# Kernel optimization log

Hardware: AMD Instinct MI355X
Metric: run time of the kernel (lower is better)

The kernel has to match this reference:

```python
import jax, jax.numpy as jnp
import numpy as np

B, P, ENC = 64, 196, 2048
A = H = E = 512
V = 30000
L = 30  # max caption length; T = L-1 decode steps


def setup_inputs() -> dict:
    key = jax.random.key(0)
    ks = jax.random.split(key, 24)
    s = 0.02
    lengths = jax.random.randint(ks[1], (B, 1), 2, L + 1)
    lengths = lengths.at[0, 0].set(L)  # ensure max length present
    return {
        "encoder_out": jax.random.normal(ks[0], (B, P, ENC), dtype=jnp.float32),
        "enc_att_w": jax.random.normal(ks[2], (A, ENC), jnp.float32) * s,
        "enc_att_b": jnp.zeros((A,), jnp.float32),
        "dec_att_w": jax.random.normal(ks[3], (A, H), jnp.float32) * s,
        "dec_att_b": jnp.zeros((A,), jnp.float32),
        "full_att_w": jax.random.normal(ks[4], (1, A), jnp.float32) * s,
        "full_att_b": jnp.zeros((1,), jnp.float32),
        "embed": jax.random.uniform(ks[5], (V, E), jnp.float32, -0.1, 0.1),
        "W_ih": jax.random.normal(ks[6], (4 * H, E + ENC), jnp.float32) * s,
        "W_hh": jax.random.normal(ks[7], (4 * H, H), jnp.float32) * s,
        "b_ih": jnp.zeros((4 * H,), jnp.float32),
        "b_hh": jnp.zeros((4 * H,), jnp.float32),
        "init_h_w": jax.random.normal(ks[8], (H, ENC), jnp.float32) * s,
        "init_h_b": jnp.zeros((H,), jnp.float32),
        "init_c_w": jax.random.normal(ks[9], (H, ENC), jnp.float32) * s,
        "init_c_b": jnp.zeros((H,), jnp.float32),
        "f_beta_w": jax.random.normal(ks[10], (ENC, H), jnp.float32) * s,
        "f_beta_b": jnp.zeros((ENC,), jnp.float32),
        "fc_w": jax.random.uniform(ks[11], (V, H), jnp.float32, -0.1, 0.1),
        "fc_b": jnp.zeros((V,), jnp.float32),
        "encoded_captions": jax.random.randint(ks[12], (B, L), 0, V),
        "caption_lengths": lengths,
    }


def reference(encoder_out, enc_att_w, enc_att_b, dec_att_w, dec_att_b, full_att_w,
              full_att_b, embed, W_ih, W_hh, b_ih, b_hh, init_h_w, init_h_b,
              init_c_w, init_c_b, f_beta_w, f_beta_b, fc_w, fc_b,
              encoded_captions, caption_lengths):
    # sort by caption length descending (as in the torch module)
    lengths = caption_lengths[:, 0]
    sort_ind = jnp.argsort(-lengths)
    lengths = lengths[sort_ind]
    enc = encoder_out[sort_ind]               # [B,P,ENC]
    caps = encoded_captions[sort_ind]         # [B,L]
    embeds = embed[caps]                      # [B,L,E]

    mean_enc = enc.mean(axis=1)
    h0 = mean_enc @ init_h_w.T + init_h_b     # [B,H]
    c0 = mean_enc @ init_c_w.T + init_c_b
    dec_len = lengths - 1
    T = caps.shape[1] - 1

    att1 = enc @ enc_att_w.T + enc_att_b      # [B,P,A] (precompute, invariant over t)

    def step(carry, emb_t):
        h, c = carry
        att2 = h @ dec_att_w.T + dec_att_b                                    # [B,A]
        e = jnp.squeeze(jax.nn.relu(att1 + att2[:, None, :]) @ full_att_w.T + full_att_b, -1)  # [B,P]
        alpha = jax.nn.softmax(e, axis=1)
        awe = jnp.einsum('bp,bpd->bd', alpha, enc)                            # [B,ENC]
        gate = jax.nn.sigmoid(h @ f_beta_w.T + f_beta_b)
        awe = gate * awe
        x = jnp.concatenate([emb_t, awe], axis=1)                             # [B,E+ENC]
        gates = x @ W_ih.T + b_ih + h @ W_hh.T + b_hh                         # [B,4H]
        i, f, g, o = jnp.split(gates, 4, axis=1)
        c_new = jax.nn.sigmoid(f) * c + jax.nn.sigmoid(i) * jnp.tanh(g)
        h_new = jax.nn.sigmoid(o) * jnp.tanh(c_new)
        preds = h_new @ fc_w.T + fc_b  # dropout in eval mode = identity
        return (h_new, c_new), (preds, alpha)

    _, (preds, alphas) = jax.lax.scan(step, (h0, c0), jnp.swapaxes(embeds[:, :T], 0, 1))
    preds = jnp.swapaxes(preds, 0, 1)   # [B,T,V]
    alphas = jnp.swapaxes(alphas, 0, 1)  # [B,T,P]
    mask = (jnp.arange(T)[None, :] < dec_len[:, None]).astype(preds.dtype)
    preds = preds * mask[:, :, None]
    alphas = alphas * mask[:, :, None]
    return preds, caps, dec_len, alphas, sort_ind
```

## Files before the change

kernel.cpp:

```cpp
#include <hip/hip_runtime.h>
#include <hip/hip_bf16.h>
#include <cstdint>

#define Bq 64
#define Pq 196
#define ENCq 2048
#define Aq 512
#define Hq 512
#define Vq 30000
#define Lq 30
#define Tq 29

typedef __bf16 bf16x8 __attribute__((ext_vector_type(8)));
typedef float f32x4 __attribute__((ext_vector_type(4)));
typedef __hip_bfloat16 bf16_t;

__device__ __forceinline__ float sigmoidf_(float x){ return 1.0f/(1.0f+expf(-x)); }

__global__ void sort_kernel(const int* __restrict__ cap_len, const int* __restrict__ caps,
                            int* __restrict__ sort_ind_i, int* __restrict__ dec_len_i,
                            int* __restrict__ caps_sorted,
                            float* __restrict__ out_caps, float* __restrict__ out_declen,
                            float* __restrict__ out_sortind)
{
    __shared__ int len[Bq];
    __shared__ int sidx[Bq];
    int i = threadIdx.x;
    len[i] = cap_len[i];
    __syncthreads();
    int li = len[i];
    int rank = 0;
    for (int j = 0; j < Bq; j++){
        int lj = len[j];
        rank += (lj > li) || (lj == li && j < i);
    }
// ... 4 lines not shown
    int dl = len[src] - 1;
    dec_len_i[i] = dl;
    out_declen[i] = (float)dl;
    out_sortind[i] = (float)src;
    for (int tt = 0; tt < Lq; tt++){
        int cv = caps[src*Lq + tt];
        caps_sorted[i*Lq + tt] = cv;
        out_caps[i*Lq + tt] = (float)cv;
    }
}

__global__ void cvt_bf16(bf16_t* __restrict__ dst, const float* __restrict__ src, int n)
{
    int i = blockIdx.x*256 + threadIdx.x;
    if (i < n) dst[i] = __float2bfloat16(src[i]);
}

__global__ void pack_rowcat_bf16(bf16_t* __restrict__ dst, const float* __restrict__ a, int na,
                                 const float* __restrict__ b, int nb)
{
    int i = blockIdx.x*256 + threadIdx.x;
    if (i < na) dst[i] = __float2bfloat16(a[i]);
    else if (i < na + nb) dst[i] = __float2bfloat16(b[i - na]);
}

__global__ void pack_rowcat_f32(float* __restrict__ dst, const float* __restrict__ a, int na,
                                const float* __restrict__ b, int nb)
{
    int i = blockIdx.x*256 + threadIdx.x;
    if (i < na) dst[i] = a[i];
    else if (i < na + nb) dst[i] = b[i - na];
}

__global__ void pack_colcat_perm_bf16(bf16_t* __restrict__ dst, const float* __restrict__ a,
                                      const float* __restrict__ b)
{
    int i = blockIdx.x*256 + threadIdx.x;
    if (i >= 2048*3072) return;
    int rp = i / 3072, c = i % 3072;
    int g = rp & 3, j = rp >> 2;
    int r = g*512 + j;
    float v = (c < 2560) ? a[(size_t)r*2560 + c] : b[(size_t)r*512 + (c - 2560)];
    dst[i] = __float2bfloat16(v);
}

__global__ void biasg_perm_kernel(float* __restrict__ dst, const float* __restrict__ bi,
                                  const float* __restrict__ bh)
{
    int i = blockIdx.x*256 + threadIdx.x;
    if (i >= 2048) return;
    int g = i & 3, j = i >> 2;
    int r = g*512 + j;
    dst[i] = bi[r] + bh[r];
}

__global__ __launch_bounds__(256)
void gather_cvt_mean(const float* __restrict__ enc, const int* __restrict__ sort_ind,
                     bf16_t* __restrict__ enc_bf, bf16_t* __restrict__ mean_bf)
{
    int b = blockIdx.x;
    int d = blockIdx.y*256 + threadIdx.x;
    int src = sort_ind[b];
    const float* col = enc + (size_t)src * Pq * ENCq + d;
    bf16_t* dst = enc_bf + (size_t)b * Pq * ENCq + d;
    float s = 0.f;
    for (int p = 0; p < Pq; p++){
        float v = col[(size_t)p*ENCq];
        s += v;
        dst[(size_t)p*ENCq] = __float2bfloat16(v);
    }
    mean_bf[(size_t)b*ENCq + d] = __float2bfloat16(s * (1.0f/196.0f));
}

__global__ __launch_bounds__(256)
void hc0_ksplit(const bf16_t* __restrict__ A, const bf16_t* __restrict__ W,
                const float* __restrict__ bias,
                bf16_t* __restrict__ h0, float* __restrict__ c_state)
{
    __shared__ float red[2][64][64];
    const int lane = threadIdx.x & 63;
    const int wave = threadIdx.x >> 6;
    const int mr = lane & 15;
    const int quad = lane >> 4;
    const int n0 = blockIdx.x * 64;
    const int kw = 2048 >> 2;
    const int kbeg = wave * kw;
// ... 96 lines not shown
    f32x4 acc[4][4];
    #pragma unroll
    for (int i = 0; i < 4; i++)
        #pragma unroll
        for (int j = 0; j < 4; j++) acc[i][j] = zero;

    for (int k = 0; k < ENCq; k += 32){
        bf16x8 a[4], b[4];
        #pragma unroll
        for (int mt = 0; mt < 4; mt++) a[mt] = *(const bf16x8*)(ap[mt] + k);
        #pragma unroll
        for (int nt = 0; nt < 4; nt++) b[nt] = *(const bf16x8*)(bp[nt] + k);
        #pragma unroll
        for (int mt = 0; mt < 4; mt++)
            #pragma unroll
            for (int nt = 0; nt < 4; nt++)
                acc[mt][nt] = __builtin_amdgcn_mfma_f32_16x16x32_bf16(a[mt], b[nt], acc[mt][nt], 0, 0, 0);
    }
    #pragma unroll
    for (int mt = 0; mt < 4; mt++){
        #pragma unroll
        for (int nt = 0; nt < 4; nt++){
            int n = n0 + nt*16 + mr;
            float bv = bias[n];
            #pragma unroll
            for (int r = 0; r < 4; r++){
                int m = m0 + mt*16 + quad*4 + r;
                C[(size_t)m*Aq + n] = __float2bfloat16(acc[mt][nt][r] + bv);
            }
        }
    }
}

__global__ __launch_bounds__(256)
void attg_gemm(const bf16_t* __restrict__ h, const bf16_t* __restrict__ W,
               const float* __restrict__ bias, float* __restrict__ C)
{
    __shared__ __bf16 hs[64][520];
    {
        int r = threadIdx.x >> 2;
        int c0 = (threadIdx.x & 3) * 128;
        const bf16_t* src = h + (size_t)r*512 + c0;
        #pragma unroll
        for (int i = 0; i < 16; i++)
            *(bf16x8*)&hs[r][c0 + i*8] = *(const bf16x8*)(src + i*8);
    }
    __syncthreads();

    const int lane = threadIdx.x & 63;
    const int wave = threadIdx.x >> 6;
    const int mr = lane & 15;
    const int quad = lane >> 4;
    const int n0 = (blockIdx.x * 4 + wave) * 16;

    const bf16_t* bp = W + (size_t)(n0 + mr)*512 + quad*8;
    f32x4 zero = {0.f,0.f,0.f,0.f};
    f32x4 acc[4] = {zero, zero, zero, zero};

    #pragma unroll
    for (int kk = 0; kk < 16; kk++){
        bf16x8 b = *(const bf16x8*)(bp + kk*32);
        bf16x8 a[4];
        #pragma unroll
        for (int mt = 0; mt < 4; mt++)
            a[mt] = *(const bf16x8*)&hs[mt*16 + mr][kk*32 + quad*8];
        #pragma unroll
        for (int mt = 0; mt < 4; mt++)
            acc[mt] = __builtin_amdgcn_mfma_f32_16x16x32_bf16(a[mt], b, acc[mt], 0, 0, 0);
    }

    float bv = bias[n0 + mr];
    #pragma unroll
    for (int mt = 0; mt < 4; mt++){
        #pragma unroll
        for (int r = 0; r < 4; r++){
            int m = mt*16 + quad*4 + r;
            C[(size_t)m*2560 + n0 + mr] = acc[mt][r] + bv;
        }
    }
}

__global__ __launch_bounds__(256)
void gates_lstm(const bf16_t* __restrict__ A, const bf16_t* __restrict__ W,
                const float* __restrict__ bias, float* __restrict__ c_state,
                bf16_t* __restrict__ h_next)
{
    __shared__ float red[2][64][64];
    const int lane = threadIdx.x & 63;
    const int wave = threadIdx.x >> 6;
    const int mr = lane & 15;
    const int quad = lane >> 4;
    const int n0 = blockIdx.x * 64;
    const int kw = 3072 >> 2;
    const int kbeg = wave * kw;

    const bf16_t* ap[4];
    const bf16_t* bp[4];
    #pragma unroll
    for (int i = 0; i < 4; i++){
        ap[i] = A + (size_t)(i*16 + mr)*3072 + quad*8;
        bp[i] = W + (size_t)(n0 + i*16 + mr)*3072 + quad*8;
    }
    f32x4 zero = {0.f,0.f,0.f,0.f};
    f32x4 acc[4][4];
    #pragma unroll
    for (int i = 0; i < 4; i++)
        #pragma unroll
        for (int j = 0; j < 4; j++) acc[i][j] = zero;

    for (int k = kbeg; k < kbeg + kw; k += 32){
        bf16x8 a[4], b[4];
        #pragma unroll
        for (int mt = 0; mt < 4; mt++) a[mt] = *(const bf16x8*)(ap[mt] + k);
        #pragma unroll
        for (int nt = 0; nt < 4; nt++) b[nt] = *(const bf16x8*)(bp[nt] + k);
        #pragma unroll
        for (int mt = 0; mt < 4; mt++)
            #pragma unroll
            for (int nt = 0; nt < 4; nt++)
                acc[mt][nt] = __builtin_amdgcn_mfma_f32_16x16x32_bf16(a[mt], b[nt], acc[mt][nt], 0, 0, 0);
    }

    if (wave >= 2){
        #pragma unroll
        for (int mt = 0; mt < 4; mt++)
            #pragma unroll
            for (int nt = 0; nt < 4; nt++)
                #pragma unroll
                for (int r = 0; r < 4; r++)
                    red[wave-2][mt*16 + quad*4 + r][nt*16 + mr] = acc[mt][nt][r];
    }
    __syncthreads();
    if (wave < 2){
        #pragma unroll
        for (int mt = 0; mt < 4; mt++)
            #pragma unroll
            for (int nt = 0; nt < 4; nt++)
                #pragma unroll
                for (int r = 0; r < 4; r++)
                    acc[mt][nt][r] += red[wave][mt*16 + quad*4 + r][nt*16 + mr];
    }
    __syncthreads();
    if (wave == 1){
        #pragma unroll
        for (int mt = 0; mt < 4; mt++)
            #pragma unroll
            for (int nt = 0; nt < 4; nt++)
                #pragma unroll
                for (int r = 0; r < 4; r++)
                    red[0][mt*16 + quad*4 + r][nt*16 + mr] = acc[mt][nt][r];
    }
    __syncthreads();
    if (wave == 0){
        #pragma unroll
        for (int mt = 0; mt < 4; mt++){
            #pragma unroll
            for (int nt = 0; nt < 4; nt++){
                int nl = nt*16 + mr;
                float bv = bias[n0 + nl];
                #pragma unroll
                for (int r = 0; r < 4; r++){
                    int m = mt*16 + quad*4 + r;
                    float v = acc[mt][nt][r] + red[0][m][nl] + bv;
                    red[0][m][nl] = v;
                }
            }
        }
    }
    __syncthreads();
    #pragma unroll
    for (int q = 0; q < 4; q++){
        int idx = threadIdx.x + 256*q;
        int m = idx & 63;
        int jl = idx >> 6;
        int j = (n0 >> 2) + jl;
        float gi = sigmoidf_(red[0][m][4*jl + 0]);
        float gf = sigmoidf_(red[0][m][4*jl + 1]);
        float gg = tanhf(red[0][m][4*jl + 2]);
        float go = sigmoidf_(red[0][m][4*jl + 3]);
        float c  = c_state[m*512 + j];
        float cn = gf*c + gi*gg;
        float hn = go * tanhf(cn);
        c_state[m*512 + j] = cn;
        h_next[m*512 + j] = __float2bfloat16(hn);
    }
}

__global__ __launch_bounds__(256)
void preds_batched(const bf16_t* __restrict__ Ah, const bf16_t* __restrict__ W,
                   const float* __restrict__ bias, float* __restrict__ C,
                   const int* __restrict__ dec_len)
{
    const int lane = threadIdx.x & 63;
    const int wave = threadIdx.x >> 6;
    const int mr = lane & 15;
    const int quad = lane >> 4;
    const int m0 = blockIdx.x * 256 + wave * 64;
    const int n0 = blockIdx.y * 64;

    const bf16_t* ap[4];
    const bf16_t* bp[4];
    #pragma unroll
    for (int i = 0; i < 4; i++){
        int row = m0 + i*16 + mr; if (row > 1855) row = 1855;
        ap[i] = Ah + (size_t)row*512 + quad*8;
        int n = n0 + i*16 + mr;   if (n > Vq-1) n = Vq-1;
        bp[i] = W + (size_t)n*512 + quad*8;
    }
    f32x4 zero = {0.f,0.f,0.f,0.f};
    f32x4 acc[4][4];
    #pragma unroll
    for (int i = 0; i < 4; i++)
        #pragma unroll
        for (int j = 0; j < 4; j++) acc[i][j] = zero;

    #pragma unroll
    for (int kk = 0; kk < 16; kk++){
        bf16x8 a[4], b[4];
        #pragma unroll
        for (int mt = 0; mt < 4; mt++) a[mt] = *(const bf16x8*)(ap[mt] + kk*32);
        #pragma unroll
        for (int nt = 0; nt < 4; nt++) b[nt] = *(const bf16x8*)(bp[nt] + kk*32);
        #pragma unroll
        for (int mt = 0; mt < 4; mt++)
            #pragma unroll
            for (int nt = 0; nt < 4; nt++)
                acc[mt][nt] = __builtin_amdgcn_mfma_f32_16x16x32_bf16(a[mt], b[nt], acc[mt][nt], 0, 0, 0);
    }

    #pragma unroll
    for (int mt = 0; mt < 4; mt++){
        #pragma unroll
        for (int r = 0; r < 4; r++){
            int m = m0 + mt*16 + quad*4 + r;
            if (m >= 1856) continue;
            int tt = m >> 6, b = m & 63;
            bool msk = (tt >= dec_len[b]);
            float* crow = C + (size_t)b*(Tq*Vq) + (size_t)tt*Vq;
            #pragma unroll
            for (int nt = 0; nt < 4; nt++){
                int n = n0 + nt*16 + mr;
                if (n < Vq){
                    float v = acc[mt][nt][r] + bias[n];
                    crow[n] = msk ? 0.f : v;
                }
            }
        }
    }
}

__global__ __launch_bounds__(256)
void attn_kernel(const bf16_t* __restrict__ att1,
                 const float* __restrict__ att2gate,
                 const float* __restrict__ faw, const float* __restrict__ fab,
                 const int* __restrict__ dec_len,
                 float* __restrict__ alpha_ws,
                 float* __restrict__ alphas_out, int t)
{
    __shared__ float es[Pq];
    __shared__ float red[8];
    int b = blockIdx.x;
    int tid = threadIdx.x;
    int wid = tid >> 6, lane = tid & 63;

    float a2r[8], fwr[8];
    {
        const float4* a2p = (const float4*)(att2gate + (size_t)b*2560);
        const float4* fwp = (const float4*)faw;
        float4 u0 = a2p[lane*2], u1 = a2p[lane*2+1];
        float4 w0 = fwp[lane*2], w1 = fwp[lane*2+1];
        a2r[0]=u0.x; a2r[1]=u0.y; a2r[2]=u0.z; a2r[3]=u0.w;
        a2r[4]=u1.x; a2r[5]=u1.y; a2r[6]=u1.z; a2r[7]=u1.w;
        fwr[0]=w0.x; fwr[1]=w0.y; fwr[2]=w0.z; fwr[3]=w0.w;
        fwr[4]=w1.x; fwr[5]=w1.y; fwr[6]=w1.z; fwr[7]=w1.w;
    }
    float fb = fab[0];
    const bf16_t* a1b = att1 + (size_t)b * Pq * Aq + lane*8;
    for (int p = wid; p < Pq; p += 4){
        bf16x8 rv = *(const bf16x8*)(a1b + (size_t)p * Aq);
        float s = 0.f;
        #pragma unroll
        for (int i = 0; i < 8; i++){
            float v = (float)rv[i] + a2r[i];
            v = v > 0.f ? v : 0.f;
            s += v * fwr[i];
        }
        #pragma unroll
        for (int off = 32; off; off >>= 1) s += __shfl_xor(s, off);
        if (lane == 0) es[p] = s + fb;
    }
    __syncthreads();
    float v = (tid < Pq) ? es[tid] : -3.4e38f;
    float m = v;
    #pragma unroll
    for (int off = 32; off; off >>= 1) m = fmaxf(m, __shfl_xor(m, off));
    if ((tid & 63) == 0) red[tid >> 6] = m;
    __syncthreads();
    float bm = fmaxf(fmaxf(red[0], red[1]), fmaxf(red[2], red[3]));
    float ex = (tid < Pq) ? expf(v - bm) : 0.f;
    float s = ex;
    #pragma unroll
    for (int off = 32; off; off >>= 1) s += __shfl_xor(s, off);
    if ((tid & 63) == 0) red[4 + (tid >> 6)] = s;
    __syncthreads();
    float bs = red[4] + red[5] + red[6] + red[7];
    if (tid < Pq){
        float al = ex / bs;
        alpha_ws[b*Pq + tid] = al;
        float mask = (t < dec_len[b]) ? 1.f : 0.f;
        alphas_out[((size_t)b*Tq + t)*Pq + tid] = al * mask;
    }
}

__global__ __launch_bounds__(256)
void awe_xcat_kernel(const bf16_t* __restrict__ enc_bf,
                     const float* __restrict__ att2gate,
                     const float* __restrict__ alpha_ws,
                     const float* __restrict__ embed,
                     const bf16_t* __restrict__ h_prev,
                     const int* __restrict__ caps_sorted,
                     bf16_t* __restrict__ xcat, int t)
{
    int b = blockIdx.x, y = blockIdx.y, tid = threadIdx.x;
    __shared__ float als[Pq];
    if (tid < Pq) als[tid] = alpha_ws[b*Pq + tid];
    __syncthreads();
    int d = y*256 + tid;
    const bf16_t* ebase = enc_bf + (size_t)b * Pq * ENCq + d;
    float s = 0.f;
    for (int p = 0; p < Pq; p++) s += als[p] * (float)ebase[(size_t)p*ENCq];
    float g = sigmoidf_(att2gate[(size_t)b*2560 + 512 + d]);
    xcat[(size_t)b*3072 + 512 + d] = __float2bfloat16(g * s);
    if (y == 0){
        int cap = caps_sorted[b*Lq + t];
        const float* er = embed + (size_t)cap*512;
        for (int j = tid; j < 512; j += 256) xcat[(size_t)b*3072 + j] = __float2bfloat16(er[j]);
    } else if (y == 1){
        for (int j = tid; j < Hq; j += 256) xcat[(size_t)b*3072 + 2560 + j] = h_prev[b*512 + j];
    }
}

extern "C" void kernel_launch(void* const* d_in, const int* in_sizes, int n_in,
                              void* d_out, int out_size, void* d_ws, size_t ws_size,
                              hipStream_t stream)
{
    const float* encoder_out = (const float*)d_in[0];
    const float* enc_att_w   = (const float*)d_in[1];
    const float* enc_att_b   = (const float*)d_in[2];
    const float* dec_att_w   = (const float*)d_in[3];
    const float* dec_att_b   = (const float*)d_in[4];
    const float* full_att_w  = (const float*)d_in[5];
    const float* full_att_b  = (const float*)d_in[6];
    const float* embed       = (const float*)d_in[7];
    const float* W_ih        = (const float*)d_in[8];
    const float* W_hh        = (const float*)d_in[9];
    const float* b_ih        = (const float*)d_in[10];
    const float* b_hh        = (const float*)d_in[11];
    const float* init_h_w    = (const float*)d_in[12];
    const float* init_h_b    = (const float*)d_in[13];
    const float* init_c_w    = (const float*)d_in[14];
    const float* init_c_b    = (const float*)d_in[15];
    const float* f_beta_w    = (const float*)d_in[16];
    const float* f_beta_b    = (const float*)d_in[17];
    const float* fc_w        = (const float*)d_in[18];
    const float* fc_b        = (const float*)d_in[19];
    const int*   enc_caps    = (const int*)d_in[20];
    const int*   cap_len     = (const int*)d_in[21];

    float* out_preds   = (float*)d_out;
    float* out_caps    = out_preds + (size_t)Bq*Tq*Vq;
    float* out_declen  = out_caps + Bq*Lq;
    float* out_alphas  = out_declen + Bq;
    float* out_sortind = out_alphas + (size_t)Bq*Tq*Pq;

    char* cur = (char*)d_ws;
    auto alloc = [&](size_t bytes) -> char* {
        char* p = cur;
        cur += (bytes + 255) & ~(size_t)255;
        return p;
    };
    bf16_t* enc_bf    = (bf16_t*)alloc((size_t)12544*2048*2);
    bf16_t* att1_bf   = (bf16_t*)alloc((size_t)12544*512*2);
    bf16_t* fcw_bf    = (bf16_t*)alloc((size_t)30000*512*2);
    bf16_t* wcatg_bf  = (bf16_t*)alloc((size_t)2048*3072*2);
    bf16_t* whc_bf    = (bf16_t*)alloc((size_t)1024*2048*2);
    bf16_t* wcat2_bf  = (bf16_t*)alloc((size_t)2560*512*2);
    bf16_t* encattw_bf= (bf16_t*)alloc((size_t)512*2048*2);
    bf16_t* meanenc_bf= (bf16_t*)alloc((size_t)64*2048*2);
    bf16_t* h_hist    = (bf16_t*)alloc((size_t)30*64*512*2);
    bf16_t* xcat_bf   = (bf16_t*)alloc((size_t)64*3072*2);
    float* c_state   = (float*)alloc((size_t)64*512*4);
    float* att2gate  = (float*)alloc((size_t)64*2560*4);
    float* bias_hc   = (float*)alloc(1024*4);
    float* bias2     = (float*)alloc(2560*4);
    float* bias_g    = (float*)alloc(2048*4);
    float* alpha_ws  = (float*)alloc((size_t)64*196*4);
    int* caps_sorted = (int*)alloc(Bq*Lq*4);
    int* sort_ind_i  = (int*)alloc(64*4);
    int* dec_len_i   = (int*)alloc(64*4);

    sort_kernel<<<1, 64, 0, stream>>>(cap_len, enc_caps, sort_ind_i, dec_len_i,
                                      caps_sorted, out_caps, out_declen, out_sortind);

    cvt_bf16<<<(1048576+255)/256, 256, 0, stream>>>(encattw_bf, enc_att_w, 1048576);
    cvt_bf16<<<(15360000+255)/256, 256, 0, stream>>>(fcw_bf, fc_w, 15360000);
    pack_rowcat_bf16<<<(2097152+255)/256, 256, 0, stream>>>(whc_bf, init_h_w, 1048576, init_c_w, 1048576);
    pack_rowcat_bf16<<<(1310720+255)/256, 256, 0, stream>>>(wcat2_bf, dec_att_w, 262144, f_beta_w, 1048576);
    pack_colcat_perm_bf16<<<(6291456+255)/256, 256, 0, stream>>>(wcatg_bf, W_ih, W_hh);
    pack_rowcat_f32<<<(1024+255)/256, 256, 0, stream>>>(bias_hc, init_h_b, 512, init_c_b, 512);
    pack_rowcat_f32<<<(2560+255)/256, 256, 0, stream>>>(bias2, dec_att_b, 512, f_beta_b, 2048);
    biasg_perm_kernel<<<8, 256, 0, stream>>>(bias_g, b_ih, b_hh);

    gather_cvt_mean<<<dim3(64,8), 256, 0, stream>>>(encoder_out, sort_ind_i, enc_bf, meanenc_bf);

    hc0_ksplit<<<16, 256, 0, stream>>>(meanenc_bf, whc_bf, bias_hc, h_hist, c_state);

    att1_gemm<<<dim3(196,2), 256, 0, stream>>>(enc_bf, encattw_bf, enc_att_b, att1_bf);

    for (int t = 0; t < Tq; t++){
        const bf16_t* h_prev = h_hist + (size_t)t*Bq*Hq;
        bf16_t* h_next = h_hist + (size_t)(t+1)*Bq*Hq;

        attg_gemm<<<40, 256, 0, stream>>>(h_prev, wcat2_bf, bias2, att2gate);

        attn_kernel<<<64, 256, 0, stream>>>(att1_bf, att2gate, full_att_w, full_att_b,
                                            dec_len_i, alpha_ws, out_alphas, t);

        awe_xcat_kernel<<<dim3(64,8), 256, 0, stream>>>(enc_bf, att2gate, alpha_ws, embed,
                                                        h_prev, caps_sorted, xcat_bf, t);

        gates_lstm<<<32, 256, 0, stream>>>(xcat_bf, wcatg_bf, bias_g, c_state, h_next);
    }

    preds_batched<<<dim3(8,469), 256, 0, stream>>>(h_hist + (size_t)Bq*Hq, fcw_bf, fc_b,
                                                   out_preds, dec_len_i);
}
```

Before: 3.117 ms.

## Fuse per-step decoder kernels into one persistent cooperative kernel with grid syncs

Replaces the four kernel launches per decode step (attention-gate GEMM, attention softmax, attention-weighted encoding, LSTM gates) with a single cooperative persistent kernel that loops over all steps and separates phases with grid-wide syncs. This removes per-step launch overhead and the att2gate scratch round trip. The att2 and f_beta projections are now scalar per-batch dot products computed inside each phase instead of an MFMA GEMM, and the gate GEMM is retiled to 16-wide column blocks across 128 blocks. The cost is redundant scalar work, reliance on grid-sync latency, and using only 64 blocks for the attention phase.

```diff
diff --git a/kernel.cpp b/kernel.cpp
--- a/kernel.cpp
+++ b/kernel.cpp
@@ -1,6 +1,9 @@
 #include <hip/hip_runtime.h>
 #include <hip/hip_bf16.h>
+#include <hip/hip_cooperative_groups.h>
 #include <cstdint>
+
+namespace cg = cooperative_groups;
 
 #define Bq 64
 #define Pq 196
@@ -253,157 +256,204 @@
     }
 }
 
-__global__ __launch_bounds__(256)
-void attg_gemm(const bf16_t* __restrict__ h, const bf16_t* __restrict__ W,
-               const float* __restrict__ bias, float* __restrict__ C)
-{
-    __shared__ __bf16 hs[64][520];
-    {
-        int r = threadIdx.x >> 2;
-        int c0 = (threadIdx.x & 3) * 128;
-        const bf16_t* src = h + (size_t)r*512 + c0;
-        #pragma unroll
-        for (int i = 0; i < 16; i++)
-            *(bf16x8*)&hs[r][c0 + i*8] = *(const bf16x8*)(src + i*8);
-    }
-    __syncthreads();
-
-    const int lane = threadIdx.x & 63;
-    const int wave = threadIdx.x >> 6;
-    const int mr = lane & 15;
-    const int quad = lane >> 4;
-    const int n0 = (blockIdx.x * 4 + wave) * 16;
-
-    const bf16_t* bp = W + (size_t)(n0 + mr)*512 + quad*8;
-    f32x4 zero = {0.f,0.f,0.f,0.f};
-    f32x4 acc[4] = {zero, zero, zero, zero};
-
-    #pragma unroll
-    for (int kk = 0; kk < 16; kk++){
-        bf16x8 b = *(const bf16x8*)(bp + kk*32);
-        bf16x8 a[4];
-        #pragma unroll
-        for (int mt = 0; mt < 4; mt++)
-            a[mt] = *(const bf16x8*)&hs[mt*16 + mr][kk*32 + quad*8];
-        #pragma unroll
-        for (int mt = 0; mt < 4; mt++)
-            acc[mt] = __builtin_amdgcn_mfma_f32_16x16x32_bf16(a[mt], b, acc[mt], 0, 0, 0);
-    }
-
-    float bv = bias[n0 + mr];
-    #pragma unroll
-    for (int mt = 0; mt < 4; mt++){
-        #pragma unroll
-        for (int r = 0; r < 4; r++){
-            int m = mt*16 + quad*4 + r;
-            C[(size_t)m*2560 + n0 + mr] = acc[mt][r] + bv;
+__global__ __launch_bounds__(256, 2)
+void loop_kernel(const bf16_t* __restrict__ att1, const bf16_t* __restrict__ wcat2,
+                 const float* __restrict__ bias2, const float* __restrict__ faw,
+                 const float* __restrict__ fab, const int* __restrict__ dec_len,
+                 float* __restrict__ alpha_ws, float* __restrict__ alphas_out,
+                 const bf16_t* __restrict__ enc_bf, const float* __restrict__ embed,
+                 const int* __restrict__ caps_sorted, bf16_t* __restrict__ xcat,
+                 const bf16_t* __restrict__ wcatg, const float* __restrict__ bias_g,
+                 float* __restrict__ c_state, bf16_t* __restrict__ h_hist)
+{
+    cg::grid_group gg = cg::this_grid();
+    const int tid = threadIdx.x;
+    const int nblk = gridDim.x;
+    const int wid = tid >> 6, lane = tid & 63;
+
+    __shared__ float hls[512];
+    __shared__ float a2s[512];
+    __shared__ float es[Pq];
+    __shared__ float redw[8];
+    __shared__ float als[Pq];
+    __shared__ float red4[2][64][17];
+
+    for (int t = 0; t < Tq; t++){
+        const bf16_t* hbase = h_hist + (size_t)t*Bq*Hq;
+
+        for (int b = blockIdx.x; b < Bq; b += nblk){
+            const bf16_t* hp = hbase + (size_t)b*Hq;
+            for (int j = tid; j < 512; j += 256) hls[j] = (float)hp[j];
+            __syncthreads();
+            #pragma unroll
+            for (int jj = 0; jj < 2; jj++){
+                int j = tid + jj*256;
+                const bf16_t* wr = wcat2 + (size_t)j*512;
+                float s = 0.f;
+                for (int k = 0; k < 512; k += 8){
+                    bf16x8 w = *(const bf16x8*)(wr + k);
+                    #pragma unroll
+                    for (int i = 0; i < 8; i++) s += hls[k+i]*(float)w[i];
+                }
+                a2s[j] = s + bias2[j];
+            }
+            __syncthreads();
+            float a2r[8], fwr[8];
+            {
+                const float4* fwp = (const float4*)faw;
+                float4 w0 = fwp[lane*2], w1 = fwp[lane*2+1];
+                fwr[0]=w0.x; fwr[1]=w0.y; fwr[2]=w0.z; fwr[3]=w0.w;
+                fwr[4]=w1.x; fwr[5]=w1.y; fwr[6]=w1.z; fwr[7]=w1.w;
+                #pragma unroll
+                for (int i = 0; i < 8; i++) a2r[i] = a2s[lane*8 + i];
+            }
+            float fb = fab[0];
+            const bf16_t* a1b = att1 + (size_t)b * Pq * Aq + lane*8;
+            for (int p = wid; p < Pq; p += 4){
+                bf16x8 rv = *(const bf16x8*)(a1b + (size_t)p * Aq);
+                float s = 0.f;
+                #pragma unroll
+                for (int i = 0; i < 8; i++){
+                    float v = (float)rv[i] + a2r[i];
+                    v = v > 0.f ? v : 0.f;
+                    s += v * fwr[i];
+                }
+                #pragma unroll
+                for (int off = 32; off; off >>= 1) s += __shfl_xor(s, off);
+                if (lane == 0) es[p] = s + fb;
+            }
+            __syncthreads();
+            float v = (tid < Pq) ? es[tid] : -3.4e38f;
+            float m = v;
+            #pragma unroll
+            for (int off = 32; off; off >>= 1) m = fmaxf(m, __shfl_xor(m, off));
+            if (lane == 0) redw[wid] = m;
+            __syncthreads();
+            float bm = fmaxf(fmaxf(redw[0], redw[1]), fmaxf(redw[2], redw[3]));
+            float ex = (tid < Pq) ? expf(v - bm) : 0.f;
+            float s2 = ex;
+            #pragma unroll
+            for (int off = 32; off; off >>= 1) s2 += __shfl_xor(s2, off);
+            if (lane == 0) redw[4 + wid] = s2;
+            __syncthreads();
+            float bs = redw[4] + redw[5] + redw[6] + redw[7];
+            if (tid < Pq){
+                float al = ex / bs;
+                alpha_ws[b*Pq + tid] = al;
+                float mask = (t < dec_len[b]) ? 1.f : 0.f;
+                alphas_out[((size_t)b*Tq + t)*Pq + tid] = al * mask;
+            }
+            __syncthreads();
         }
-    }
-}
-
-__global__ __launch_bounds__(256)
-void gates_lstm(const bf16_t* __restrict__ A, const bf16_t* __restrict__ W,
-                const float* __restrict__ bias, float* __restrict__ c_state,
-                bf16_t* __restrict__ h_next)
-{
-    __shared__ float red[2][64][64];
-    const int lane = threadIdx.x & 63;
-    const int wave = threadIdx.x >> 6;
-    const int mr = lane & 15;
-    const int quad = lane >> 4;
-    const int n0 = blockIdx.x * 64;
-    const int kw = 3072 >> 2;
-    const int kbeg = wave * kw;
-
-    const bf16_t* ap[4];
-    const bf16_t* bp[4];
-    #pragma unroll
-    for (int i = 0; i < 4; i++){
-        ap[i] = A + (size_t)(i*16 + mr)*3072 + quad*8;
-        bp[i] = W + (size_t)(n0 + i*16 + mr)*3072 + quad*8;
-    }
-    f32x4 zero = {0.f,0.f,0.f,0.f};
-    f32x4 acc[4][4];
-    #pragma unroll
-    for (int i = 0; i < 4; i++)
-        #pragma unroll
-        for (int j = 0; j < 4; j++) acc[i][j] = zero;
-
-    for (int k = kbeg; k < kbeg + kw; k += 32){
-        bf16x8 a[4], b[4];
-        #pragma unroll
-        for (int mt = 0; mt < 4; mt++) a[mt] = *(const bf16x8*)(ap[mt] + k);
-        #pragma unroll
-        for (int nt = 0; nt < 4; nt++) b[nt] = *(const bf16x8*)(bp[nt] + k);
-        #pragma unroll
-        for (int mt = 0; mt < 4; mt++)
-            #pragma unroll
-            for (int nt = 0; nt < 4; nt++)
-                acc[mt][nt] = __builtin_amdgcn_mfma_f32_16x16x32_bf16(a[mt], b[nt], acc[mt][nt], 0, 0, 0);
-    }
-
-    if (wave >= 2){
-        #pragma unroll
-        for (int mt = 0; mt < 4; mt++)
-            #pragma unroll
-            for (int nt = 0; nt < 4; nt++)
-                #pragma unroll
-                for (int r = 0; r < 4; r++)
-                    red[wave-2][mt*16 + quad*4 + r][nt*16 + mr] = acc[mt][nt][r];
-    }
-    __syncthreads();
-    if (wave < 2){
-        #pragma unroll
-        for (int mt = 0; mt < 4; mt++)
-            #pragma unroll
-            for (int nt = 0; nt < 4; nt++)
-                #pragma unroll
-                for (int r = 0; r < 4; r++)
-                    acc[mt][nt][r] += red[wave][mt*16 + quad*4 + r][nt*16 + mr];
-    }
-    __syncthreads();
-    if (wave == 1){
-        #pragma unroll
-        for (int mt = 0; mt < 4; mt++)
-            #pragma unroll
-            for (int nt = 0; nt < 4; nt++)
-                #pragma unroll
-                for (int r = 0; r < 4; r++)
-                    red[0][mt*16 + quad*4 + r][nt*16 + mr] = acc[mt][nt][r];
-    }
-    __syncthreads();
-    if (wave == 0){
-        #pragma unroll
-        for (int mt = 0; mt < 4; mt++){
-            #pragma unroll
-            for (int nt = 0; nt < 4; nt++){
-                int nl = nt*16 + mr;
-                float bv = bias[n0 + nl];
-                #pragma unroll
-                for (int r = 0; r < 4; r++){
-                    int m = mt*16 + quad*4 + r;
-                    float v = acc[mt][nt][r] + red[0][m][nl] + bv;
-                    red[0][m][nl] = v;
+        gg.sync();
+
+        for (int c = blockIdx.x; c < Bq*8; c += nblk){
+            int b = c >> 3, q = c & 7;
+            const bf16_t* hp = hbase + (size_t)b*Hq;
+            if (tid < Pq) als[tid] = alpha_ws[b*Pq + tid];
+            for (int j = tid; j < 512; j += 256) hls[j] = (float)hp[j];
+            __syncthreads();
+            int d = q*256 + tid;
+            const bf16_t* eb = enc_bf + (size_t)b * Pq * ENCq + d;
+            float s = 0.f;
+            #pragma unroll 4
+            for (int p = 0; p < Pq; p++) s += als[p] * (float)eb[(size_t)p*ENCq];
+            const bf16_t* wr = wcat2 + (size_t)(512 + d)*512;
+            float gs = 0.f;
+            for (int k = 0; k < 512; k += 8){
+                bf16x8 w = *(const bf16x8*)(wr + k);
+                #pragma unroll
+                for (int i = 0; i < 8; i++) gs += hls[k+i]*(float)w[i];
+            }
+            float g = sigmoidf_(gs + bias2[512 + d]);
+            xcat[(size_t)b*3072 + 512 + d] = __float2bfloat16(g * s);
+            if (q == 0){
+                int cap = caps_sorted[b*Lq + t];
+                const float* er = embed + (size_t)cap*512;
+                for (int j = tid; j < 512; j += 256)
+                    xcat[(size_t)b*3072 + j] = __float2bfloat16(er[j]);
+            } else if (q == 1){
+                for (int j = tid; j < 512; j += 256)
+                    xcat[(size_t)b*3072 + 2560 + j] = hp[j];
+            }
+            __syncthreads();
+        }
+        gg.sync();
+
+        for (int nb = blockIdx.x; nb < 128; nb += nblk){
+            const int mr = lane & 15;
+            const int quad = lane >> 4;
+            const int n0 = nb * 16;
+            const int kbeg = wid * 768;
+
+            const bf16_t* ap[4];
+            #pragma unroll
+            for (int i = 0; i < 4; i++) ap[i] = xcat + (size_t)(i*16 + mr)*3072 + quad*8;
+            const bf16_t* bp = wcatg + (size_t)(n0 + mr)*3072 + quad*8;
+
+            f32x4 zero = {0.f,0.f,0.f,0.f};
+            f32x4 acc[4] = {zero, zero, zero, zero};
+            for (int k = kbeg; k < kbeg + 768; k += 32){
+                bf16x8 bfr = *(const bf16x8*)(bp + k);
+                bf16x8 a[4];
+                #pragma unroll
+                for (int mt = 0; mt < 4; mt++) a[mt] = *(const bf16x8*)(ap[mt] + k);
+                #pragma unroll
+                for (int mt = 0; mt < 4; mt++)
+                    acc[mt] = __builtin_amdgcn_mfma_f32_16x16x32_bf16(a[mt], bfr, acc[mt], 0, 0, 0);
+            }
+            if (wid >= 2){
+                #pragma unroll
+                for (int mt = 0; mt < 4; mt++)
+                    #pragma unroll
+                    for (int r = 0; r < 4; r++)
+                        red4[wid-2][mt*16 + quad*4 + r][mr] = acc[mt][r];
+            }
+            __syncthreads();
+            if (wid < 2){
+                #pragma unroll
+                for (int mt = 0; mt < 4; mt++)
+                    #pragma unroll
+                    for (int r = 0; r < 4; r++)
+                        acc[mt][r] += red4[wid][mt*16 + quad*4 + r][mr];
+            }
+            __syncthreads();
+            if (wid == 1){
+                #pragma unroll
+                for (int mt = 0; mt < 4; mt++)
+                    #pragma unroll
+                    for (int r = 0; r < 4; r++)
+                        red4[0][mt*16 + quad*4 + r][mr] = acc[mt][r];
+            }
+            __syncthreads();
+            if (wid == 0){
+                float bv = bias_g[n0 + mr];
+                #pragma unroll
+                for (int mt = 0; mt < 4; mt++){
+                    #pragma unroll
+                    for (int r = 0; r < 4; r++){
+                        int m = mt*16 + quad*4 + r;
+                        red4[0][m][mr] = acc[mt][r] + red4[0][m][mr] + bv;
+                    }
                 }
             }
+            __syncthreads();
+            {
+                int m = tid & 63, jl = tid >> 6;
+                int j = nb*4 + jl;
+                float gi = sigmoidf_(red4[0][m][4*jl + 0]);
+                float gf = sigmoidf_(red4[0][m][4*jl + 1]);
+                float gv = tanhf(red4[0][m][4*jl + 2]);
+                float go = sigmoidf_(red4[0][m][4*jl + 3]);
+                float cc = c_state[m*512 + j];
+                float cn = gf*cc + gi*gv;
+                float hn = go * tanhf(cn);
+                c_state[m*512 + j] = cn;
+                h_hist[(size_t)(t+1)*Bq*Hq + m*512 + j] = __float2bfloat16(hn);
+            }
+            __syncthreads();
         }
-    }
-    __syncthreads();
-    #pragma unroll
-    for (int q = 0; q < 4; q++){
-        int idx = threadIdx.x + 256*q;
-        int m = idx & 63;
-        int jl = idx >> 6;
-        int j = (n0 >> 2) + jl;
-        float gi = sigmoidf_(red[0][m][4*jl + 0]);
-        float gf = sigmoidf_(red[0][m][4*jl + 1]);
-        float gg = tanhf(red[0][m][4*jl + 2]);
-        float go = sigmoidf_(red[0][m][4*jl + 3]);
-        float c  = c_state[m*512 + j];
-        float cn = gf*c + gi*gg;
-        float hn = go * tanhf(cn);
-        c_state[m*512 + j] = cn;
-        h_next[m*512 + j] = __float2bfloat16(hn);
+        gg.sync();
     }
 }
 
@@ -467,97 +517,6 @@
                 }
             }
         }
-    }
-}
-
-__global__ __launch_bounds__(256)
-void attn_kernel(const bf16_t* __restrict__ att1,
-                 const float* __restrict__ att2gate,
-                 const float* __restrict__ faw, const float* __restrict__ fab,
-                 const int* __restrict__ dec_len,
-                 float* __restrict__ alpha_ws,
-                 float* __restrict__ alphas_out, int t)
-{
-    __shared__ float es[Pq];
-    __shared__ float red[8];
-    int b = blockIdx.x;
-    int tid = threadIdx.x;
-    int wid = tid >> 6, lane = tid & 63;
-
-    float a2r[8], fwr[8];
-    {
-        const float4* a2p = (const float4*)(att2gate + (size_t)b*2560);
-        const float4* fwp = (const float4*)faw;
-        float4 u0 = a2p[lane*2], u1 = a2p[lane*2+1];
-        float4 w0 = fwp[lane*2], w1 = fwp[lane*2+1];
-        a2r[0]=u0.x; a2r[1]=u0.y; a2r[2]=u0.z; a2r[3]=u0.w;
-        a2r[4]=u1.x; a2r[5]=u1.y; a2r[6]=u1.z; a2r[7]=u1.w;
-        fwr[0]=w0.x; fwr[1]=w0.y; fwr[2]=w0.z; fwr[3]=w0.w;
-        fwr[4]=w1.x; fwr[5]=w1.y; fwr[6]=w1.z; fwr[7]=w1.w;
-    }
-    float fb = fab[0];
-    const bf16_t* a1b = att1 + (size_t)b * Pq * Aq + lane*8;
-    for (int p = wid; p < Pq; p += 4){
-        bf16x8 rv = *(const bf16x8*)(a1b + (size_t)p * Aq);
-        float s = 0.f;
-        #pragma unroll
-        for (int i = 0; i < 8; i++){
-            float v = (float)rv[i] + a2r[i];
-            v = v > 0.f ? v : 0.f;
-            s += v * fwr[i];
-        }
-        #pragma unroll
-        for (int off = 32; off; off >>= 1) s += __shfl_xor(s, off);
-        if (lane == 0) es[p] = s + fb;
-    }
-    __syncthreads();
-    float v = (tid < Pq) ? es[tid] : -3.4e38f;
-    float m = v;
-    #pragma unroll
-    for (int off = 32; off; off >>= 1) m = fmaxf(m, __shfl_xor(m, off));
-    if ((tid & 63) == 0) red[tid >> 6] = m;
-    __syncthreads();
-    float bm = fmaxf(fmaxf(red[0], red[1]), fmaxf(red[2], red[3]));
-    float ex = (tid < Pq) ? expf(v - bm) : 0.f;
-    float s = ex;
-    #pragma unroll
-    for (int off = 32; off; off >>= 1) s += __shfl_xor(s, off);
-    if ((tid & 63) == 0) red[4 + (tid >> 6)] = s;
-    __syncthreads();
-    float bs = red[4] + red[5] + red[6] + red[7];
-    if (tid < Pq){
-        float al = ex / bs;
-        alpha_ws[b*Pq + tid] = al;
-        float mask = (t < dec_len[b]) ? 1.f : 0.f;
-        alphas_out[((size_t)b*Tq + t)*Pq + tid] = al * mask;
-    }
-}
-
-__global__ __launch_bounds__(256)
-void awe_xcat_kernel(const bf16_t* __restrict__ enc_bf,
-                     const float* __restrict__ att2gate,
-                     const float* __restrict__ alpha_ws,
-                     const float* __restrict__ embed,
-                     const bf16_t* __restrict__ h_prev,
-                     const int* __restrict__ caps_sorted,
-                     bf16_t* __restrict__ xcat, int t)
-{
-    int b = blockIdx.x, y = blockIdx.y, tid = threadIdx.x;
-    __shared__ float als[Pq];
-    if (tid < Pq) als[tid] = alpha_ws[b*Pq + tid];
-    __syncthreads();
-    int d = y*256 + tid;
-    const bf16_t* ebase = enc_bf + (size_t)b * Pq * ENCq + d;
-    float s = 0.f;
-    for (int p = 0; p < Pq; p++) s += als[p] * (float)ebase[(size_t)p*ENCq];
-    float g = sigmoidf_(att2gate[(size_t)b*2560 + 512 + d]);
-    xcat[(size_t)b*3072 + 512 + d] = __float2bfloat16(g * s);
-    if (y == 0){
-        int cap = caps_sorted[b*Lq + t];
-        const float* er = embed + (size_t)cap*512;
-        for (int j = tid; j < 512; j += 256) xcat[(size_t)b*3072 + j] = __float2bfloat16(er[j]);
-    } else if (y == 1){
-        for (int j = tid; j < Hq; j += 256) xcat[(size_t)b*3072 + 2560 + j] = h_prev[b*512 + j];
     }
 }
 
@@ -611,7 +570,6 @@
     bf16_t* h_hist    = (bf16_t*)alloc((size_t)30*64*512*2);
     bf16_t* xcat_bf   = (bf16_t*)alloc((size_t)64*3072*2);
     float* c_state   = (float*)alloc((size_t)64*512*4);
-    float* att2gate  = (float*)alloc((size_t)64*2560*4);
     float* bias_hc   = (float*)alloc(1024*4);
     float* bias2     = (float*)alloc(2560*4);
     float* bias_g    = (float*)alloc(2048*4);
@@ -638,19 +596,20 @@
 
     att1_gemm<<<dim3(196,2), 256, 0, stream>>>(enc_bf, encattw_bf, enc_att_b, att1_bf);
 
-    for (int t = 0; t < Tq; t++){
-        const bf16_t* h_prev = h_hist + (size_t)t*Bq*Hq;
-        bf16_t* h_next = h_hist + (size_t)(t+1)*Bq*Hq;
-
-        attg_gemm<<<40, 256, 0, stream>>>(h_prev, wcat2_bf, bias2, att2gate);
-
-        attn_kernel<<<64, 256, 0, stream>>>(att1_bf, att2gate, full_att_w, full_att_b,
-                                            dec_len_i, alpha_ws, out_alphas, t);
-
-        awe_xcat_kernel<<<dim3(64,8), 256, 0, stream>>>(enc_bf, att2gate, alpha_ws, embed,
-                                                        h_prev, caps_sorted, xcat_bf, t);
-
-        gates_lstm<<<32, 256, 0, stream>>>(xcat_bf, wcatg_bf, bias_g, c_state, h_next);
+    static int coop_blocks = 0;
+    if (coop_blocks == 0){
+        int occ = 0;
+        if (hipOccupancyMaxActiveBlocksPerMultiprocessor(&occ, (const void*)loop_kernel, 256, 0) != hipSuccess || occ < 1)
+            occ = 1;
+        coop_blocks = occ >= 2 ? 512 : 256;
+    }
+    {
+        void* cargs[] = { (void*)&att1_bf, (void*)&wcat2_bf, (void*)&bias2, (void*)&full_att_w,
+                          (void*)&full_att_b, (void*)&dec_len_i, (void*)&alpha_ws, (void*)&out_alphas,
+                          (void*)&enc_bf, (void*)&embed, (void*)&caps_sorted, (void*)&xcat_bf,
+                          (void*)&wcatg_bf, (void*)&bias_g, (void*)&c_state, (void*)&h_hist };
+        hipLaunchCooperativeKernel((const void*)loop_kernel, dim3(coop_blocks), dim3(256),
+                                   cargs, 0, stream);
     }
 
     preds_batched<<<dim3(8,469), 256, 0, stream>>>(h_hist + (size_t)Bq*Hq, fcw_bf, fc_b,
```

After: 8.986 ms. +188.3%, slower.

## Precompute embedding gate projections for all steps and shrink per-step LSTM GEMM

Applied to the files above, without the earlier changes.

The embedding part of the LSTM input projection no longer runs inside the recurrence. Embeddings for every timestep are gathered and multiplied by the W_ih embedding columns in one batched GEMM before the loop. Each step's gates kernel then handles only the K=2560 attention-weighted-encoding and hidden part, and the output columns are split across 128 blocks of 16 instead of 32 blocks of 64, giving more parallelism on the serial path. The preds GEMM swaps its MFMA operands so each lane writes four contiguous floats with float4 stores. The cost is an extra fp32 gate buffer that every step must read.

```diff
diff --git a/kernel.cpp b/kernel.cpp
--- a/kernel.cpp
+++ b/kernel.cpp
@@ -71,16 +71,26 @@
     else if (i < na + nb) dst[i] = b[i - na];
 }
 
-__global__ void pack_colcat_perm_bf16(bf16_t* __restrict__ dst, const float* __restrict__ a,
-                                      const float* __restrict__ b)
+__global__ void pack_wcatg2(bf16_t* __restrict__ dst, const float* __restrict__ wih,
+                            const float* __restrict__ whh)
 {
     int i = blockIdx.x*256 + threadIdx.x;
-    if (i >= 2048*3072) return;
-    int rp = i / 3072, c = i % 3072;
+    if (i >= 2048*2560) return;
+    int rp = i / 2560, c = i % 2560;
     int g = rp & 3, j = rp >> 2;
     int r = g*512 + j;
-    float v = (c < 2560) ? a[(size_t)r*2560 + c] : b[(size_t)r*512 + (c - 2560)];
+    float v = (c < 2048) ? wih[(size_t)r*2560 + 512 + c] : whh[(size_t)r*512 + (c - 2048)];
     dst[i] = __float2bfloat16(v);
+}
+
+__global__ void pack_wembg(bf16_t* __restrict__ dst, const float* __restrict__ wih)
+{
+    int i = blockIdx.x*256 + threadIdx.x;
+    if (i >= 2048*512) return;
+    int rp = i >> 9, c = i & 511;
+    int g = rp & 3, j = rp >> 2;
+    int r = g*512 + j;
+    dst[i] = __float2bfloat16(wih[(size_t)r*2560 + c]);
 }
 
 __global__ void biasg_perm_kernel(float* __restrict__ dst, const float* __restrict__ bi,
@@ -91,6 +101,17 @@
     int g = i & 3, j = i >> 2;
     int r = g*512 + j;
     dst[i] = bi[r] + bh[r];
+}
+
+__global__ void gather_emb(const float* __restrict__ embed, const int* __restrict__ caps_sorted,
+                           bf16_t* __restrict__ embA)
+{
+    int m = blockIdx.x;
+    int t = m >> 6, b = m & 63;
+    int cap = caps_sorted[b*Lq + t];
+    const float* er = embed + (size_t)cap*512;
+    bf16_t* dr = embA + (size_t)m*512;
+    for (int j = threadIdx.x; j < 512; j += 256) dr[j] = __float2bfloat16(er[j]);
 }
 
 __global__ __launch_bounds__(256)
@@ -254,6 +275,58 @@
 }
 
 __global__ __launch_bounds__(256)
+void embg_gemm(const bf16_t* __restrict__ A, const bf16_t* __restrict__ W,
+               float* __restrict__ C)
+{
+    const int lane = threadIdx.x & 63;
+    const int wave = threadIdx.x >> 6;
+    const int mr = lane & 15;
+    const int quad = lane >> 4;
+    const int m0 = blockIdx.x * 64;
+    const int n0 = (blockIdx.y * 4 + wave) * 64;
+
+    const bf16_t* ap[4];
+    const bf16_t* bp[4];
+    #pragma unroll
+    for (int i = 0; i < 4; i++){
+        ap[i] = A + (size_t)(m0 + i*16 + mr)*512 + quad*8;
+        bp[i] = W + (size_t)(n0 + i*16 + mr)*512 + quad*8;
+    }
+    f32x4 zero = {0.f,0.f,0.f,0.f};
+    f32x4 acc[4][4];
+    #pragma unroll
+    for (int i = 0; i < 4; i++)
+        #pragma unroll
+        for (int j = 0; j < 4; j++) acc[i][j] = zero;
+
+    #pragma unroll
+    for (int kk = 0; kk < 16; kk++){
+        bf16x8 a[4], b[4];
+        #pragma unroll
+        for (int mt = 0; mt < 4; mt++) a[mt] = *(const bf16x8*)(ap[mt] + kk*32);
+        #pragma unroll
+        for (int nt = 0; nt < 4; nt++) b[nt] = *(const bf16x8*)(bp[nt] + kk*32);
+        #pragma unroll
+        for (int mt = 0; mt < 4; mt++)
+            #pragma unroll
+            for (int nt = 0; nt < 4; nt++)
+                acc[mt][nt] = __builtin_amdgcn_mfma_f32_16x16x32_bf16(a[mt], b[nt], acc[mt][nt], 0, 0, 0);
+    }
+    #pragma unroll
+    for (int mt = 0; mt < 4; mt++){
+        #pragma unroll
+        for (int nt = 0; nt < 4; nt++){
+            int n = n0 + nt*16 + mr;
+            #pragma unroll
+            for (int r = 0; r < 4; r++){
+                int m = m0 + mt*16 + quad*4 + r;
+                C[(size_t)m*2048 + n] = acc[mt][nt][r];
+            }
+        }
+    }
+}
+
+__global__ __launch_bounds__(256)
 void attg_gemm(const bf16_t* __restrict__ h, const bf16_t* __restrict__ W,
                const float* __restrict__ bias, float* __restrict__ C)
 {
@@ -302,105 +375,80 @@
 }
 
 __global__ __launch_bounds__(256)
-void gates_lstm(const bf16_t* __restrict__ A, const bf16_t* __restrict__ W,
-                const float* __restrict__ bias, float* __restrict__ c_state,
-                bf16_t* __restrict__ h_next)
-{
-    __shared__ float red[2][64][64];
+void gates_lstm2(const bf16_t* __restrict__ A, const bf16_t* __restrict__ W,
+                 const float* __restrict__ bias, const float* __restrict__ gE,
+                 float* __restrict__ c_state, bf16_t* __restrict__ h_next)
+{
+    __shared__ float red4[2][64][17];
     const int lane = threadIdx.x & 63;
-    const int wave = threadIdx.x >> 6;
+    const int wid  = threadIdx.x >> 6;
     const int mr = lane & 15;
     const int quad = lane >> 4;
-    const int n0 = blockIdx.x * 64;
-    const int kw = 3072 >> 2;
-    const int kbeg = wave * kw;
+    const int n0 = blockIdx.x * 16;
+    const int kbeg = wid * 640;
 
     const bf16_t* ap[4];
-    const bf16_t* bp[4];
-    #pragma unroll
-    for (int i = 0; i < 4; i++){
-        ap[i] = A + (size_t)(i*16 + mr)*3072 + quad*8;
-        bp[i] = W + (size_t)(n0 + i*16 + mr)*3072 + quad*8;
-    }
+    #pragma unroll
+    for (int i = 0; i < 4; i++) ap[i] = A + (size_t)(i*16 + mr)*2560 + quad*8;
+    const bf16_t* bp = W + (size_t)(n0 + mr)*2560 + quad*8;
+
     f32x4 zero = {0.f,0.f,0.f,0.f};
-    f32x4 acc[4][4];
-    #pragma unroll
-    for (int i = 0; i < 4; i++)
-        #pragma unroll
-        for (int j = 0; j < 4; j++) acc[i][j] = zero;
-
-    for (int k = kbeg; k < kbeg + kw; k += 32){
-        bf16x8 a[4], b[4];
+    f32x4 acc[4] = {zero, zero, zero, zero};
+    for (int k = kbeg; k < kbeg + 640; k += 32){
+        bf16x8 bfr = *(const bf16x8*)(bp + k);
+        bf16x8 a[4];
         #pragma unroll
         for (int mt = 0; mt < 4; mt++) a[mt] = *(const bf16x8*)(ap[mt] + k);
         #pragma unroll
-        for (int nt = 0; nt < 4; nt++) b[nt] = *(const bf16x8*)(bp[nt] + k);
-        #pragma unroll
-        for (int mt = 0; mt < 4; mt++)
-            #pragma unroll
-            for (int nt = 0; nt < 4; nt++)
-                acc[mt][nt] = __builtin_amdgcn_mfma_f32_16x16x32_bf16(a[mt], b[nt], acc[mt][nt], 0, 0, 0);
-    }
-
-    if (wave >= 2){
-        #pragma unroll
-        for (int mt = 0; mt < 4; mt++)
-            #pragma unroll
-            for (int nt = 0; nt < 4; nt++)
-                #pragma unroll
-                for (int r = 0; r < 4; r++)
-                    red[wave-2][mt*16 + quad*4 + r][nt*16 + mr] = acc[mt][nt][r];
-    }
-    __syncthreads();
-    if (wave < 2){
-        #pragma unroll
-        for (int mt = 0; mt < 4; mt++)
-            #pragma unroll
-            for (int nt = 0; nt < 4; nt++)
-                #pragma unroll
-                for (int r = 0; r < 4; r++)
-                    acc[mt][nt][r] += red[wave][mt*16 + quad*4 + r][nt*16 + mr];
-    }
-    __syncthreads();
-    if (wave == 1){
-        #pragma unroll
-        for (int mt = 0; mt < 4; mt++)
-            #pragma unroll
-            for (int nt = 0; nt < 4; nt++)
-                #pragma unroll
-                for (int r = 0; r < 4; r++)
-                    red[0][mt*16 + quad*4 + r][nt*16 + mr] = acc[mt][nt][r];
-    }
-    __syncthreads();
-    if (wave == 0){
+        for (int mt = 0; mt < 4; mt++)
+            acc[mt] = __builtin_amdgcn_mfma_f32_16x16x32_bf16(a[mt], bfr, acc[mt], 0, 0, 0);
+    }
+    if (wid >= 2){
+        #pragma unroll
+        for (int mt = 0; mt < 4; mt++)
+            #pragma unroll
+            for (int r = 0; r < 4; r++)
+                red4[wid-2][mt*16 + quad*4 + r][mr] = acc[mt][r];
+    }
+    __syncthreads();
+    if (wid < 2){
+        #pragma unroll
+        for (int mt = 0; mt < 4; mt++)
+            #pragma unroll
+            for (int r = 0; r < 4; r++)
+                acc[mt][r] += red4[wid][mt*16 + quad*4 + r][mr];
+    }
+    __syncthreads();
+    if (wid == 1){
+        #pragma unroll
+        for (int mt = 0; mt < 4; mt++)
+            #pragma unroll
+            for (int r = 0; r < 4; r++)
+                red4[0][mt*16 + quad*4 + r][mr] = acc[mt][r];
+    }
+    __syncthreads();
+    if (wid == 0){
+        float bv = bias[n0 + mr];
         #pragma unroll
         for (int mt = 0; mt < 4; mt++){
             #pragma unroll
-            for (int nt = 0; nt < 4; nt++){
-                int nl = nt*16 + mr;
-                float bv = bias[n0 + nl];
-                #pragma unroll
-                for (int r = 0; r < 4; r++){
-                    int m = mt*16 + quad*4 + r;
-                    float v = acc[mt][nt][r] + red[0][m][nl] + bv;
-                    red[0][m][nl] = v;
-                }
+            for (int r = 0; r < 4; r++){
+                int m = mt*16 + quad*4 + r;
+                float ge = gE[(size_t)m*2048 + n0 + mr];
+                red4[0][m][mr] = acc[mt][r] + red4[0][m][mr] + bv + ge;
             }
         }
     }
     __syncthreads();
-    #pragma unroll
-    for (int q = 0; q < 4; q++){
-        int idx = threadIdx.x + 256*q;
-        int m = idx & 63;
-        int jl = idx >> 6;
-        int j = (n0 >> 2) + jl;
-        float gi = sigmoidf_(red[0][m][4*jl + 0]);
-        float gf = sigmoidf_(red[0][m][4*jl + 1]);
-        float gg = tanhf(red[0][m][4*jl + 2]);
-        float go = sigmoidf_(red[0][m][4*jl + 3]);
-        float c  = c_state[m*512 + j];
-        float cn = gf*c + gi*gg;
+    {
+        int m = threadIdx.x & 63, jl = threadIdx.x >> 6;
+        int j = blockIdx.x*4 + jl;
+        float gi = sigmoidf_(red4[0][m][4*jl + 0]);
+        float gf = sigmoidf_(red4[0][m][4*jl + 1]);
+        float gv = tanhf(red4[0][m][4*jl + 2]);
+        float go = sigmoidf_(red4[0][m][4*jl + 3]);
+        float cc = c_state[m*512 + j];
+        float cn = gf*cc + gi*gv;
         float hn = go * tanhf(cn);
         c_state[m*512 + j] = cn;
         h_next[m*512 + j] = __float2bfloat16(hn);
@@ -446,25 +494,28 @@
         for (int mt = 0; mt < 4; mt++)
             #pragma unroll
             for (int nt = 0; nt < 4; nt++)
-                acc[mt][nt] = __builtin_amdgcn_mfma_f32_16x16x32_bf16(a[mt], b[nt], acc[mt][nt], 0, 0, 0);
+                acc[mt][nt] = __builtin_amdgcn_mfma_f32_16x16x32_bf16(b[nt], a[mt], acc[mt][nt], 0, 0, 0);
     }
 
     #pragma unroll
     for (int mt = 0; mt < 4; mt++){
-        #pragma unroll
-        for (int r = 0; r < 4; r++){
-            int m = m0 + mt*16 + quad*4 + r;
-            if (m >= 1856) continue;
-            int tt = m >> 6, b = m & 63;
-            bool msk = (tt >= dec_len[b]);
-            float* crow = C + (size_t)b*(Tq*Vq) + (size_t)tt*Vq;
-            #pragma unroll
-            for (int nt = 0; nt < 4; nt++){
-                int n = n0 + nt*16 + mr;
-                if (n < Vq){
-                    float v = acc[mt][nt][r] + bias[n];
-                    crow[n] = msk ? 0.f : v;
-                }
+        int m = m0 + mt*16 + mr;
+        if (m >= 1856) continue;
+        int tt = m >> 6, b = m & 63;
+        bool msk = (tt >= dec_len[b]);
+        float* crow = C + (size_t)b*(Tq*Vq) + (size_t)tt*Vq;
+        #pragma unroll
+        for (int nt = 0; nt < 4; nt++){
+            int n = n0 + nt*16 + quad*4;
+            if (n < Vq){
+                float4 bv = *(const float4*)(bias + n);
+                f32x4 v = acc[mt][nt];
+                float4 o;
+                o.x = msk ? 0.f : (v[0] + bv.x);
+                o.y = msk ? 0.f : (v[1] + bv.y);
+                o.z = msk ? 0.f : (v[2] + bv.z);
+                o.w = msk ? 0.f : (v[3] + bv.w);
+                *(float4*)(crow + n) = o;
             }
         }
     }
@@ -534,13 +585,11 @@
 }
 
 __global__ __launch_bounds__(256)
-void awe_xcat_kernel(const bf16_t* __restrict__ enc_bf,
-                     const float* __restrict__ att2gate,
-                     const float* __restrict__ alpha_ws,
-                     const float* __restrict__ embed,
-                     const bf16_t* __restrict__ h_prev,
-                     const int* __restrict__ caps_sorted,
-                     bf16_t* __restrict__ xcat, int t)
+void awe_xcat2(const bf16_t* __restrict__ enc_bf,
+               const float* __restrict__ att2gate,
+               const float* __restrict__ alpha_ws,
+               const bf16_t* __restrict__ h_prev,
+               bf16_t* __restrict__ xcat2)
 {
     int b = blockIdx.x, y = blockIdx.y, tid = threadIdx.x;
     __shared__ float als[Pq];
@@ -549,15 +598,13 @@
     int d = y*256 + tid;
     const bf16_t* ebase = enc_bf + (size_t)b * Pq * ENCq + d;
     float s = 0.f;
+    #pragma unroll 4
     for (int p = 0; p < Pq; p++) s += als[p] * (float)ebase[(size_t)p*ENCq];
     float g = sigmoidf_(att2gate[(size_t)b*2560 + 512 + d]);
-    xcat[(size_t)b*3072 + 512 + d] = __float2bfloat16(g * s);
+    xcat2[(size_t)b*2560 + d] = __float2bfloat16(g * s);
     if (y == 0){
-        int cap = caps_sorted[b*Lq + t];
-        const float* er = embed + (size_t)cap*512;
-        for (int j = tid; j < 512; j += 256) xcat[(size_t)b*3072 + j] = __float2bfloat16(er[j]);
-    } else if (y == 1){
-        for (int j = tid; j < Hq; j += 256) xcat[(size_t)b*3072 + 2560 + j] = h_prev[b*512 + j];
+        for (int j = tid; j < 512; j += 256)
+            xcat2[(size_t)b*2560 + 2048 + j] = h_prev[b*512 + j];
     }
 }
 
@@ -603,13 +650,16 @@
     bf16_t* enc_bf    = (bf16_t*)alloc((size_t)12544*2048*2);
     bf16_t* att1_bf   = (bf16_t*)alloc((size_t)12544*512*2);
     bf16_t* fcw_bf    = (bf16_t*)alloc((size_t)30000*512*2);
-    bf16_t* wcatg_bf  = (bf16_t*)alloc((size_t)2048*3072*2);
+    bf16_t* wcatg_bf  = (bf16_t*)alloc((size_t)2048*2560*2);
+    bf16_t* wembg_bf  = (bf16_t*)alloc((size_t)2048*512*2);
+    bf16_t* embA_bf   = (bf16_t*)alloc((size_t)1856*512*2);
+    float*  gatesE    = (float*)alloc((size_t)1856*2048*4);
     bf16_t* whc_bf    = (bf16_t*)alloc((size_t)1024*2048*2);
     bf16_t* wcat2_bf  = (bf16_t*)alloc((size_t)2560*512*2);
     bf16_t* encattw_bf= (bf16_t*)alloc((size_t)512*2048*2);
     bf16_t* meanenc_bf= (bf16_t*)alloc((size_t)64*2048*2);
     bf16_t* h_hist    = (bf16_t*)alloc((size_t)30*64*512*2);
-    bf16_t* xcat_bf   = (bf16_t*)alloc((size_t)64*3072*2);
+    bf16_t* xcat2_bf  = (bf16_t*)alloc((size_t)64*2560*2);
     float* c_state   = (float*)alloc((size_t)64*512*4);
     float* att2gate  = (float*)alloc((size_t)64*2560*4);
     float* bias_hc   = (float*)alloc(1024*4);
@@ -627,11 +677,15 @@
     cvt_bf16<<<(15360000+255)/256, 256, 0, stream>>>(fcw_bf, fc_w, 15360000);
     pack_rowcat_bf16<<<(2097152+255)/256, 256, 0, stream>>>(whc_bf, init_h_w, 1048576, init_c_w, 1048576);
     pack_rowcat_bf16<<<(1310720+255)/256, 256, 0, stream>>>(wcat2_bf, dec_att_w, 262144, f_beta_w, 1048576);
-    pack_colcat_perm_bf16<<<(6291456+255)/256, 256, 0, stream>>>(wcatg_bf, W_ih, W_hh);
+    pack_wcatg2<<<(2048*2560+255)/256, 256, 0, stream>>>(wcatg_bf, W_ih, W_hh);
+    pack_wembg<<<(2048*512+255)/256, 256, 0, stream>>>(wembg_bf, W_ih);
     pack_rowcat_f32<<<(1024+255)/256, 256, 0, stream>>>(bias_hc, init_h_b, 512, init_c_b, 512);
     pack_rowcat_f32<<<(2560+255)/256, 256, 0, stream>>>(bias2, dec_att_b, 512, f_beta_b, 2048);
     biasg_perm_kernel<<<8, 256, 0, stream>>>(bias_g, b_ih, b_hh);
 
+    gather_emb<<<1856, 256, 0, stream>>>(embed, caps_sorted, embA_bf);
+    embg_gemm<<<dim3(29,8), 256, 0, stream>>>(embA_bf, wembg_bf, gatesE);
+
     gather_cvt_mean<<<dim3(64,8), 256, 0, stream>>>(encoder_out, sort_ind_i, enc_bf, meanenc_bf);
 
     hc0_ksplit<<<16, 256, 0, stream>>>(meanenc_bf, whc_bf, bias_hc, h_hist, c_state);
@@ -647,10 +701,10 @@
         attn_kernel<<<64, 256, 0, stream>>>(att1_bf, att2gate, full_att_w, full_att_b,
                                             dec_len_i, alpha_ws, out_alphas, t);
 
-        awe_xcat_kernel<<<dim3(64,8), 256, 0, stream>>>(enc_bf, att2gate, alpha_ws, embed,
-                                                        h_prev, caps_sorted, xcat_bf, t);
-
-        gates_lstm<<<32, 256, 0, stream>>>(xcat_bf, wcatg_bf, bias_g, c_state, h_next);
+        awe_xcat2<<<dim3(64,8), 256, 0, stream>>>(enc_bf, att2gate, alpha_ws, h_prev, xcat2_bf);
+
+        gates_lstm2<<<128, 256, 0, stream>>>(xcat2_bf, wcatg_bf, bias_g,
+                                             gatesE + (size_t)t*64*2048, c_state, h_next);
     }
 
     preds_batched<<<dim3(8,469), 256, 0, stream>>>(h_hist + (size_t)Bq*Hq, fcw_bf, fc_b,
```

Result: faster. 3.005 ms (-3.6%).
